# Kernel optimization log

Measured on AMD Instinct MI355X. Metric: run time of the kernel, lower is better.

The kernel has to match this reference:

```python
import jax, jax.numpy as jnp
import numpy as np

B, NQ, NK, C = 16, 8, 4096, 256
H = W = 64
HEADS = 8
CI = 128          # embedding_dim // attention_downsample_rate
HD = CI // HEADS  # per-head dim
EPS = float(np.finfo(np.float32).tiny)


def _gumbel_topk(scores, noise, n):
    # iterative gumbel-softmax top-k relaxation with straight-through hard k-hot
    g = scores + noise
    khot = jnp.zeros_like(g)
    onehot = jnp.zeros_like(g)
    for _ in range(n):
        g = g + jnp.log(jnp.maximum(1.0 - onehot, EPS))
        onehot = jax.nn.softmax(g, axis=-1)
        khot = khot + onehot
    _, ind = jax.lax.top_k(khot, n)
    rows = jnp.arange(khot.shape[0])[:, None]
    hard = jnp.zeros_like(khot).at[rows, ind].set(1.0)
    ret = hard - jax.lax.stop_gradient(khot) + khot  # == hard numerically
    return ret, jnp.sort(ind, axis=1)  # sorted idx = row-major order of boolean-mask select


def _sample_points(pe, content, ret, idx):
    # pe [H,W,C], content [b,H,W,C], ret [b,HW] k-hot, idx [b,k] sorted
    b = ret.shape[0]
    m = ret.reshape(b, H, W, 1)
    pe_m = (pe[None] * m).reshape(b, H * W, -1)
    c_m = (content * m).reshape(b, H * W, -1)
    take = lambda a: jnp.take_along_axis(a, idx[:, :, None], axis=1)
    return take(pe_m), take(c_m)


def _mlp(x, W1, b1, W2, b2, W3, b3):
    x = jax.nn.relu(x @ W1 + b1)
    x = jax.nn.relu(x @ W2 + b2)
    return x @ W3 + b3


def _forward(queries, keys, query_pe, key_pe, guiding_embedding, gumbel_p, gumbel_n,
             static_uncertain, static_refined, Wq, bq, Wk, bk, Wv, bv, Wo, bo,
             uW1, ub1, uW2, ub2, uW3, ub3, rW1, rb1, rW2, rb2, rW3, rb3,
             pe_gauss, point_pos, point_neg, n_sample_points):
    b = queries.shape[0]
    g = guiding_embedding.reshape(b, C, H * W).transpose(0, 2, 1)  # [b, HW, C]
    g = g * keys  # elementwise gating -> new guiding embedding

    # cross attention token -> image (internal dim CI, HEADS heads)
    def split_heads(x, Wx, bx):
        return (x @ Wx + bx).reshape(b, -1, HEADS, HD).transpose(0, 2, 1, 3)
    qh = split_heads(queries + query_pe, Wq, bq)
    kh = split_heads(g + key_pe, Wk, bk)
    vh = split_heads(g, Wv, bv)
    attn = jax.nn.softmax(jnp.einsum('bhqd,bhkd->bhqk', qh, kh) / np.float32(np.sqrt(HD)), axis=-1)
    out = jnp.einsum('bhqk,bhkd->bhqd', attn, vh).transpose(0, 2, 1, 3).reshape(b, -1, CI)
    queries = out @ Wo + bo  # [b, NQ, C]

    q1 = queries[:, 1, :]
    unc_tok = _mlp(jnp.concatenate([jnp.broadcast_to(static_uncertain, (b, C)), q1], -1),
                   uW1, ub1, uW2, ub2, uW3, ub3)
    ref_tok = _mlp(jnp.concatenate([jnp.broadcast_to(static_refined, (b, C)), q1], -1),
                   rW1, rb1, rW2, rb2, rW3, rb3)

    img = g.transpose(0, 2, 1)  # [b, C, HW]
    unc_norm = jax.nn.sigmoid(jnp.einsum('bc,bcn->bn', unc_tok, img))
    ref_mask = jnp.einsum('bc,bcn->bn', ref_tok, img)
    coarse_mask = jnp.einsum('bc,bcn->bn', q1, img)

    queries = jnp.concatenate([queries[:, 0:1], ref_tok[:, None, :], queries[:, 2:]], axis=1)

    # point-sampling reference map + gumbel-softmax top-k (training-path math)
    ref_map = unc_norm * (jax.nn.sigmoid(ref_mask) - jax.nn.sigmoid(coarse_mask))  # [b, HW]
    ret_p, idx_p = _gumbel_topk(ref_map, gumbel_p, n_sample_points)
    ret_n, idx_n = _gumbel_topk(-ref_map, gumbel_n, n_sample_points)

    # random fourier positional encoding of the 64x64 grid (SAM PositionEmbeddingRandom)
    xs = (jnp.arange(W, dtype=jnp.float32) + 0.5) / W
    ys = (jnp.arange(H, dtype=jnp.float32) + 0.5) / H
    coords = jnp.stack([jnp.tile(xs[None, :], (H, 1)), jnp.tile(ys[:, None], (1, W))], axis=-1)
    proj = ((2.0 * coords - 1.0) @ pe_gauss) * np.float32(2.0 * np.pi)  # [H, W, C//2]
    pe = jnp.concatenate([jnp.sin(proj), jnp.cos(proj)], axis=-1)       # [H, W, C]

    # F.interpolate of a 64x64 map to (64,64) is the identity here
    content = (keys + g).reshape(b, H, W, C)

    sp_pe, sp_c = _sample_points(pe, content, ret_p, idx_p)
    sn_pe, sn_c = _sample_points(pe, content, ret_n, idx_n)
    sp_pe = sp_pe + point_pos  # prompt_encoder.point_embeddings[1]
    sn_pe = sn_pe + point_neg  # prompt_encoder.point_embeddings[0]

    query_pe = jnp.concatenate([query_pe, sp_pe, sn_pe], axis=1)
    queries = jnp.concatenate([queries, sp_c, sn_c], axis=1)
    # pack (queries, query_pe) into one array for a single-output reference
    return jnp.concatenate([queries, query_pe], axis=1)  # [b, 2*(NQ+2k), C]


def setup_inputs():
    key = jax.random.key(0)
    ks = iter(jax.random.split(key, 48))
    n = lambda shape, s=1.0: jax.random.normal(next(ks), shape, jnp.float32) * s
    z = lambda shape: jnp.zeros(shape, jnp.float32)
    return {
        'queries': n((B, NQ, C)),
        'keys': n((B, NK, C)),
        'query_pe': n((B, NQ, C)),
        'key_pe': n((B, NK, C)),
        'guiding_embedding': n((B, C, H, W)),
        'gumbel_p': jax.random.gumbel(next(ks), (B, NK), jnp.float32),
        'gumbel_n': jax.random.gumbel(next(ks), (B, NK), jnp.float32),
        'static_uncertain': n((C,), 0.02),
        'static_refined': n((C,), 0.02),
        'Wq': n((C, CI), 0.02), 'bq': z((CI,)),
        'Wk': n((C, CI), 0.02), 'bk': z((CI,)),
        'Wv': n((C, CI), 0.02), 'bv': z((CI,)),
        'Wo': n((CI, C), 0.02), 'bo': z((C,)),
        'uW1': n((2 * C, C // 4), 0.05), 'ub1': z((C // 4,)),
        'uW2': n((C // 4, C // 4), 0.05), 'ub2': z((C // 4,)),
        'uW3': n((C // 4, C), 0.05), 'ub3': z((C,)),
        'rW1': n((2 * C, C // 4), 0.05), 'rb1': z((C // 4,)),
        'rW2': n((C // 4, C // 4), 0.05), 'rb2': z((C // 4,)),
        'rW3': n((C // 4, C), 0.05), 'rb3': z((C,)),
        'pe_gauss': n((2, C // 2)),
        'point_pos': n((C,), 0.02),
        'point_neg': n((C,), 0.02),
        'n_sample_points': 4,
    }


def reference(queries, keys, query_pe, key_pe, guiding_embedding, gumbel_p, gumbel_n,
              static_uncertain, static_refined, Wq, bq, Wk, bk, Wv, bv, Wo, bo,
              uW1, ub1, uW2, ub2, uW3, ub3, rW1, rb1, rW2, rb2, rW3, rb3,
              pe_gauss, point_pos, point_neg, n_sample_points):
    return _forward(queries, keys, query_pe, key_pe, guiding_embedding, gumbel_p, gumbel_n,
                    static_uncertain, static_refined, Wq, bq, Wk, bk, Wv, bv, Wo, bo,
                    uW1, ub1, uW2, ub2, uW3, ub3, rW1, rb1, rW2, rb2, rW3, rb3,
                    pe_gauss, point_pos, point_neg, n_sample_points)
```

## Files before the change

kernel.cpp:

```cpp
#include <hip/hip_runtime.h>

#define BB 16
#define NQn 8
#define NK 4096
#define CC 256
#define NHEADS 8
#define CIn 128
#define HDn 16
#define NHQ 64
#define EPS_TINY 1.17549435e-38f

constexpr size_t OFF_QK   = 0;
constexpr size_t OFF_QBK  = OFF_QK  + (size_t)BB*CC*NHQ;
constexpr size_t OFF_SC   = OFF_QBK + (size_t)BB*NHQ;
constexpr size_t OFF_MP   = OFF_SC  + (size_t)BB*NK*NHQ;
constexpr size_t OFF_SP   = OFF_MP  + (size_t)BB*32*NHQ;
constexpr size_t OFF_M    = OFF_SP  + (size_t)BB*32*NHQ;
constexpr size_t OFF_RS   = OFF_M   + (size_t)BB*NHQ;
constexpr size_t OFF_AVP  = OFF_RS  + (size_t)BB*NHQ;
constexpr size_t OFF_QATT = OFF_AVP + (size_t)BB*16*NHQ*CC;
constexpr size_t OFF_UNC  = OFF_QATT+ (size_t)BB*NQn*CC;
constexpr size_t OFF_REFT = OFF_UNC + (size_t)BB*CC;
constexpr size_t OFF_RMAP = OFF_REFT+ (size_t)BB*CC;
constexpr size_t OFF_IDX  = OFF_RMAP+ (size_t)BB*NK;
constexpr size_t OFF_RV   = OFF_IDX + 128;
constexpr size_t OFF_G    = OFF_RV  + 128;

__global__ __launch_bounds__(256) void k1_qside(
    const float* __restrict__ queries, const float* __restrict__ query_pe,
    const float* __restrict__ Wq, const float* __restrict__ bq,
    const float* __restrict__ Wk, const float* __restrict__ bk,
    float* __restrict__ ws)
{
  int b = blockIdx.x >> 3, q = blockIdx.x & 7, t = threadIdx.x;
  __shared__ float x[CC];
  __shared__ float qh[CIn];
  x[t] = queries[(b*NQn+q)*CC + t] + query_pe[(b*NQn+q)*CC + t];
  __syncthreads();
  if (t < CIn) {
    float a = bq[t];
    for (int c = 0; c < CC; ++c) a += x[c]*Wq[c*CIn + t];
    qh[t] = a * 0.25f;
  }
  __syncthreads();
  float* Qk = ws + OFF_QK;
  #pragma unroll
  for (int h = 0; h < NHEADS; ++h) {
    float a = 0.f;
    #pragma unroll
    for (int d = 0; d < HDn; ++d) a += qh[h*HDn+d] * Wk[t*CIn + h*HDn + d];
    Qk[((size_t)b*CC + t)*NHQ + h*NQn + q] = a;
  }
  if (t < NHEADS) {
    float a = 0.f;
    #pragma unroll
    for (int d = 0; d < HDn; ++d) a += qh[t*HDn+d] * bk[t*HDn+d];
    (ws + OFF_QBK)[b*NHQ + t*NQn + q] = a;
  }
}

__global__ __launch_bounds__(256, 8) void k2_scores(
    const float* __restrict__ keys, const float* __restrict__ key_pe,
    const float* __restrict__ guiding, float* __restrict__ ws)
{
  int b = blockIdx.y, n0 = blockIdx.x * 32, t = threadIdx.x;
  __shared__ __align__(16) float Xs[32][36];
  __shared__ __align__(16) float Qs[32][64];
  __shared__ float Gt[32][33];
  const float* Qk = ws + OFF_QK + (size_t)b*CC*NHQ;
  float* G = ws + OFF_G;
  const int tx = t & 15, ty = t >> 4;
  const int xr = t >> 3, xc4 = (t & 7) * 4;
  const int gn = t & 31, gc0 = (t >> 5) * 4;
  float acc[2][4] = {};

  float gld[4]; float4 kp, pp; float qp[8];
  {
    #pragma unroll
    for (int i = 0; i < 4; ++i)
      gld[i] = guiding[((size_t)b*CC + gc0 + i)*NK + n0 + gn];
    size_t kb = ((size_t)b*NK + n0 + xr)*CC + xc4;
    kp = *(const float4*)&keys[kb];
    pp = *(const float4*)&key_pe[kb];
    #pragma unroll
    for (int i = 0; i < 8; ++i) {
      int l = i*256 + t;
      qp[i] = Qk[(size_t)(l>>6)*NHQ + (l & 63)];
    }
  }
  for (int ch = 0; ch < 8; ++ch) {
    int c0 = ch*32;
    #pragma unroll
    for (int i = 0; i < 4; ++i) Gt[gc0 + i][gn] = gld[i];
    __syncthreads();
    #pragma unroll
    for (int i = 0; i < 8; ++i) {
      int l = i*256 + t;
      Qs[l>>6][l&63] = qp[i];
    }
    {
      size_t kbase = ((size_t)b*NK + n0 + xr)*CC + c0 + xc4;
      float4 g4;
      g4.x = kp.x * Gt[xc4+0][xr];
      g4.y = kp.y * Gt[xc4+1][xr];
      g4.z = kp.z * Gt[xc4+2][xr];
      g4.w = kp.w * Gt[xc4+3][xr];
      *(float4*)&G[kbase] = g4;
      float4 o; o.x=g4.x+pp.x; o.y=g4.y+pp.y; o.z=g4.z+pp.z; o.w=g4.w+pp.w;
      *(float4*)&Xs[xr][xc4] = o;
    }
    __syncthreads();
    if (ch < 7) {
      int c1 = c0 + 32;
      #pragma unroll
      for (int i = 0; i < 4; ++i)
        gld[i] = guiding[((size_t)b*CC + c1 + gc0 + i)*NK + n0 + gn];
      size_t kb2 = ((size_t)b*NK + n0 + xr)*CC + c1 + xc4;
      kp = *(const float4*)&keys[kb2];
      pp = *(const float4*)&key_pe[kb2];
      #pragma unroll
      for (int i = 0; i < 8; ++i) {
        int l = i*256 + t;
        qp[i] = Qk[(size_t)(c1 + (l>>6))*NHQ + (l & 63)];
      }
    }
    #pragma unroll
    for (int cb = 0; cb < 8; ++cb) {
      float4 x0 = *(const float4*)&Xs[2*ty][4*cb];
      float4 x1 = *(const float4*)&Xs[2*ty+1][4*cb];
      #pragma unroll
      for (int u = 0; u < 4; ++u) {
        float4 qf = *(const float4*)&Qs[4*cb+u][4*tx];
        float xu0 = ((const float*)&x0)[u];
        float xu1 = ((const float*)&x1)[u];
        acc[0][0] += xu0*qf.x; acc[0][1] += xu0*qf.y; acc[0][2] += xu0*qf.z; acc[0][3] += xu0*qf.w;
        acc[1][0] += xu1*qf.x; acc[1][1] += xu1*qf.y; acc[1][2] += xu1*qf.z; acc[1][3] += xu1*qf.w;
      }
    }
  }
  const float* qbk = ws + OFF_QBK + (size_t)b*NHQ;
  float qb[4] = {qbk[4*tx], qbk[4*tx+1], qbk[4*tx+2], qbk[4*tx+3]};
  float* sc = ws + OFF_SC + ((size_t)b*NK + n0)*NHQ;
  #pragma unroll
  for (int i = 0; i < 2; ++i) {
    float4 o;
    o.x = acc[i][0]+qb[0]; o.y = acc[i][1]+qb[1]; o.z = acc[i][2]+qb[2]; o.w = acc[i][3]+qb[3];
    *(float4*)&sc[(size_t)(2*ty + i)*NHQ + 4*tx] = o;
  }
}

__global__ __launch_bounds__(256) void k3a_stats(float* __restrict__ ws)
{
  int b = blockIdx.y, sb = blockIdx.x, t = threadIdx.x;
  int hq = t & 63, r = t >> 6;
  const float* sc = ws + OFF_SC + ((size_t)b*NK + sb*128)*NHQ;
  float m = -INFINITY, s = 0.f;
  for (int i = 0; i < 32; ++i) {
    float v = sc[(r + 4*i)*NHQ + hq];
    if (v > m) { s = s*expf(m - v) + 1.f; m = v; } else { s += expf(v - m); }
  }
  __shared__ float rm[256], rs[256];
  rm[t] = m; rs[t] = s;
  __syncthreads();
  if (t < 64) {
    float m0=rm[t], m1=rm[t+64], m2=rm[t+128], m3=rm[t+192];
    float mm = fmaxf(fmaxf(m0,m1), fmaxf(m2,m3));
    float ss = rs[t]*expf(m0-mm) + rs[t+64]*expf(m1-mm) + rs[t+128]*expf(m2-mm) + rs[t+192]*expf(m3-mm);
    (ws + OFF_MP)[(b*32 + sb)*NHQ + t] = mm;
    (ws + OFF_SP)[(b*32 + sb)*NHQ + t] = ss;
  }
}

__global__ __launch_bounds__(64) void k3b_combine(float* __restrict__ ws)
{
  int b = blockIdx.x, hq = threadIdx.x;
  const float* mp = ws + OFF_MP + (size_t)b*32*NHQ;
  const float* sp = ws + OFF_SP + (size_t)b*32*NHQ;
  float m = -INFINITY;
  #pragma unroll
  for (int i = 0; i < 32; ++i) m = fmaxf(m, mp[i*NHQ+hq]);
  float s = 0.f;
  #pragma unroll
  for (int i = 0; i < 32; ++i) s += sp[i*NHQ+hq]*expf(mp[i*NHQ+hq]-m);
  (ws+OFF_M)[b*NHQ+hq] = m;
  (ws+OFF_RS)[b*NHQ+hq] = 1.0f/s;
}

__global__ __launch_bounds__(256) void k3c_weights(float* __restrict__ ws)
{
  int b = blockIdx.y, t = threadIdx.x;
  size_t f = (size_t)blockIdx.x * 2048 + (size_t)t * 8;
  float* sc = ws + OFF_SC + (size_t)b*NK*NHQ + f;
  const float* m  = ws + OFF_M  + (size_t)b*NHQ;
  const float* rs = ws + OFF_RS + (size_t)b*NHQ;
  int hq0 = (int)(f & 63);
  float4 v0 = *(const float4*)&sc[0];
  float4 v1 = *(const float4*)&sc[4];
  float o[8] = {v0.x,v0.y,v0.z,v0.w, v1.x,v1.y,v1.z,v1.w};
  #pragma unroll
  for (int j = 0; j < 8; ++j) o[j] = expf(o[j] - m[hq0+j]) * rs[hq0+j];
  float4 w0; w0.x=o[0]; w0.y=o[1]; w0.z=o[2]; w0.w=o[3];
  float4 w1; w1.x=o[4]; w1.y=o[5]; w1.z=o[6]; w1.w=o[7];
  *(float4*)&sc[0] = w0;
  *(float4*)&sc[4] = w1;
}

__global__ __launch_bounds__(256, 8) void k4_av(float* __restrict__ ws)
{
  int xb = blockIdx.x, cq = blockIdx.y, b = blockIdx.z, t = threadIdx.x;
  int kb = xb >> 1, hh = (xb & 1) * 32;
  int k0 = kb * 256, cbase = cq * 64;
  __shared__ __align__(16) float gld[32][68];
  __shared__ __align__(16) float wld[32][36];
  const int hq0 = (t & 7) * 4, c0 = (t >> 3) * 2;
  const int sr = t >> 4, sc4 = (t & 15) * 4;
  float acc[4][2] = {};
  const float* Wp = ws + OFF_SC;
  const float* G  = ws + OFF_G;
  for (int kk = 0; kk < 256; kk += 32) {
    __syncthreads();
    #pragma unroll
    for (int p = 0; p < 2; ++p)
      *(float4*)&gld[p*16 + sr][sc4] =
        *(const float4*)&G[((size_t)b*NK + k0+kk + p*16 + sr)*CC + cbase + sc4];
    #pragma unroll
    for (int i = 0; i < 4; ++i) {
      int l = i*256 + t; int k = l >> 5, hqw = l & 31;
      wld[k][hqw] = Wp[((size_t)b*NK + k0+kk+k)*NHQ + hh + hqw];
    }
    __syncthreads();
    #pragma unroll 4
    for (int k = 0; k < 32; ++k) {
      float4 w4 = *(const float4*)&wld[k][hq0];
      float2 g2 = *(const float2*)&gld[k][c0];
      acc[0][0] += w4.x*g2.x; acc[0][1] += w4.x*g2.y;
      acc[1][0] += w4.y*g2.x; acc[1][1] += w4.y*g2.y;
      acc[2][0] += w4.z*g2.x; acc[2][1] += w4.z*g2.y;
      acc[3][0] += w4.w*g2.x; acc[3][1] += w4.w*g2.y;
    }
  }
  float* avp = ws + OFF_AVP + (((size_t)b*16 + kb)*NHQ + hh + hq0)*CC + cbase + c0;
  #pragma unroll
  for (int i = 0; i < 4; ++i)
    *(float2*)&avp[(size_t)i*CC] = make_float2(acc[i][0], acc[i][1]);
}

__global__ __launch_bounds__(256) void k56_attout(
    const float* __restrict__ Wv, const float* __restrict__ bv,
    const float* __restrict__ Wo, const float* __restrict__ bo,
    float* __restrict__ ws)
{
  int b = blockIdx.x >> 3, q = blockIdx.x & 7, t = threadIdx.x;
  __shared__ float avs[NHEADS][CC];
  __shared__ float outv[CIn];
  const float* avp = ws + OFF_AVP;
  #pragma unroll
  for (int h = 0; h < NHEADS; ++h) {
    int hq = h*NQn + q;
    float a = 0.f;
    #pragma unroll 4
    for (int kb = 0; kb < 16; ++kb)
      a += avp[(((size_t)b*16 + kb)*NHQ + hq)*CC + t];
    avs[h][t] = a;
  }
  __syncthreads();
  if (t < CIn) {
    int h = t >> 4;
    float a = bv[t];
    for (int c = 0; c < CC; ++c) a += avs[h][c]*Wv[c*CIn + t];
    outv[t] = a;
  }
  __syncthreads();
  float a = bo[t];
  for (int ci = 0; ci < CIn; ++ci) a += outv[ci]*Wo[ci*CC + t];
  (ws+OFF_QATT)[((size_t)b*NQn + q)*CC + t] = a;
}

__global__ __launch_bounds__(256) void k7_mlps(
    const float* __restrict__ su, const float* __restrict__ sr,
    const float* __restrict__ uW1, const float* __restrict__ ub1,
    const float* __restrict__ uW2, const float* __restrict__ ub2,
    const float* __restrict__ uW3, const float* __restrict__ ub3,
    const float* __restrict__ rW1, const float* __restrict__ rb1,
    const float* __restrict__ rW2, const float* __restrict__ rb2,
    const float* __restrict__ rW3, const float* __restrict__ rb3,
    float* __restrict__ ws)
{
  int b = blockIdx.x, t = threadIdx.x;
  __shared__ float xs[768];
  __shared__ float h1[2][64], h2[2][64];
  xs[t] = su[t];
  xs[256+t] = (ws+OFF_QATT)[((size_t)b*NQn + 1)*CC + t];
  xs[512+t] = sr[t];
  __syncthreads();
  if (t < 128) {
    int which = t >> 6, o = t & 63;
    const float* W1 = which ? rW1 : uW1;
    const float* b1 = which ? rb1 : ub1;
    int base = which ? 512 : 0;
    float a = b1[o];
    for (int i = 0; i < 256; ++i) a += xs[base+i]*W1[i*64 + o];
    for (int i = 0; i < 256; ++i) a += xs[256+i]*W1[(256+i)*64 + o];
    h1[which][o] = fmaxf(a, 0.f);
  }
  __syncthreads();
  if (t < 128) {
    int which = t >> 6, o = t & 63;
    const float* W2 = which ? rW2 : uW2;
    const float* b2 = which ? rb2 : ub2;
    float a = b2[o];
    #pragma unroll 8
    for (int i = 0; i < 64; ++i) a += h1[which][i]*W2[i*64+o];
    h2[which][o] = fmaxf(a, 0.f);
  }
  __syncthreads();
  {
    float a = ub3[t];
    #pragma unroll 8
    for (int i = 0; i < 64; ++i) a += h2[0][i]*uW3[i*CC + t];
    (ws+OFF_UNC)[b*CC + t] = a;
    float a2 = rb3[t];
    #pragma unroll 8
    for (int i = 0; i < 64; ++i) a2 += h2[1][i]*rW3[i*CC + t];
    (ws+OFF_REFT)[b*CC + t] = a2;
  }
}

__global__ __launch_bounds__(256) void k8_masks(float* __restrict__ ws)
{
  int b = blockIdx.y, t = threadIdx.x;
  int wave = t >> 6, lane = t & 63;
  __shared__ float q1s[CC], us[CC], rts[CC];
  q1s[t] = (ws+OFF_QATT)[((size_t)b*NQn+1)*CC + t];
  us[t]  = (ws+OFF_UNC)[b*CC + t];
  rts[t] = (ws+OFF_REFT)[b*CC + t];
  __syncthreads();
  float q1v[4], usv[4], rtv[4];
  #pragma unroll
  for (int u = 0; u < 4; ++u) {
    q1v[u] = q1s[lane*4+u]; usv[u] = us[lane*4+u]; rtv[u] = rts[lane*4+u];
  }
  const float* G = ws + OFF_G;
  float* rmap = ws + OFF_RMAP + (size_t)b*NK;
  int n_base = blockIdx.x*32 + wave*8;
  for (int r = 0; r < 8; ++r) {
    int n = n_base + r;
    float4 gv = *(const float4*)&G[((size_t)b*NK + n)*CC + lane*4];
    float aq = gv.x*q1v[0] + gv.y*q1v[1] + gv.z*q1v[2] + gv.w*q1v[3];
    float au = gv.x*usv[0] + gv.y*usv[1] + gv.z*usv[2] + gv.w*usv[3];
    float ar = gv.x*rtv[0] + gv.y*rtv[1] + gv.z*rtv[2] + gv.w*rtv[3];
    #pragma unroll
    for (int s = 1; s < 64; s <<= 1) {
      aq += __shfl_xor(aq, s, 64);
      au += __shfl_xor(au, s, 64);
      ar += __shfl_xor(ar, s, 64);
    }
    if (lane == 0) {
      float un = 1.f/(1.f+expf(-au));
      rmap[n] = un * (1.f/(1.f+expf(-ar)) - 1.f/(1.f+expf(-aq)));
    }
  }
}

__global__ __launch_bounds__(256) void k9_gumbel(
    const float* __restrict__ gp, const float* __restrict__ gn,
    float* __restrict__ ws)
{
  int sign = blockIdx.x, b = blockIdx.y, t = threadIdx.x;
  int wave = t >> 6, lane = t & 63;
  const float* noise = sign ? gn : gp;
  const float* rmap = ws + OFF_RMAP + (size_t)b*NK;
  float g[16], kh[16], oh[16];
  #pragma unroll
  for (int i = 0; i < 16; ++i) {
    int n = i*256 + t;
    float scv = rmap[n];
    if (sign) scv = -scv;
    g[i] = scv + noise[(size_t)b*NK + n];
    kh[i] = 0.f; oh[i] = 0.f;
  }
  __shared__ float wred[8];
  __shared__ float selV[16];
  __shared__ int   selIdx[16];
  for (int it = 0; it < 4; ++it) {
    if (it > 0) {
      #pragma unroll
      for (int i = 0; i < 16; ++i) g[i] += logf(fmaxf(1.f - oh[i], EPS_TINY));
    }
    float m = g[0];
    #pragma unroll
    for (int i = 1; i < 16; ++i) m = fmaxf(m, g[i]);
    #pragma unroll
    for (int s = 1; s < 64; s <<= 1) m = fmaxf(m, __shfl_xor(m, s, 64));
    if (lane == 0) wred[wave] = m;
    __syncthreads();
    m = fmaxf(fmaxf(wred[0], wred[1]), fmaxf(wred[2], wred[3]));
    float e[16], ls = 0.f;
    #pragma unroll
    for (int i = 0; i < 16; ++i) { e[i] = expf(g[i]-m); ls += e[i]; }
    #pragma unroll
    for (int s = 1; s < 64; s <<= 1) ls += __shfl_xor(ls, s, 64);
    if (lane == 0) wred[4+wave] = ls;
    __syncthreads();
    float ssum = wred[4]+wred[5]+wred[6]+wred[7];
    #pragma unroll
    for (int i = 0; i < 16; ++i) { oh[i] = e[i]/ssum; kh[i] += oh[i]; }
  }
  int id[4]; float rr[4];
  for (int j = 0; j < 4; ++j) {
    float bv = kh[0]; int bi = t;
    #pragma unroll
    for (int i = 1; i < 16; ++i) {
      if (kh[i] > bv) { bv = kh[i]; bi = i*256 + t; }
    }
    #pragma unroll
    for (int s = 1; s < 64; s <<= 1) {
      float ov = __shfl_xor(bv, s, 64);
      int   oi = __shfl_xor(bi, s, 64);
      if (ov > bv || (ov == bv && oi < bi)) { bv = ov; bi = oi; }
    }
    if (lane == 0) { selV[j*4+wave] = bv; selIdx[j*4+wave] = bi; }
    __syncthreads();
    bv = selV[j*4]; bi = selIdx[j*4];
    #pragma unroll
    for (int w = 1; w < 4; ++w) {
      float ov = selV[j*4+w]; int oi = selIdx[j*4+w];
      if (ov > bv || (ov == bv && oi < bi)) { bv = ov; bi = oi; }
    }
    id[j] = bi; rr[j] = (1.f - bv) + bv;
    if ((bi & 255) == t) kh[bi >> 8] = -1.f;
  }
  if (t == 0) {
    for (int a = 0; a < 3; ++a)
      for (int c2 = a+1; c2 < 4; ++c2)
        if (id[c2] < id[a]) { int ti=id[a]; id[a]=id[c2]; id[c2]=ti; float tr=rr[a]; rr[a]=rr[c2]; rr[c2]=tr; }
    int* iout = (int*)(ws + OFF_IDX);
    float* rout = ws + OFF_RV;
    for (int j = 0; j < 4; ++j) {
      iout[(sign*BB + b)*4 + j] = id[j];
      rout[(sign*BB + b)*4 + j] = rr[j];
    }
  }
}

__global__ __launch_bounds__(256) void k10_out(
    const float* __restrict__ keys, const float* __restrict__ query_pe,
    const float* __restrict__ point_pos, const float* __restrict__ point_neg,
    const float* __restrict__ pe_gauss,
    float* __restrict__ ws, float* __restrict__ out)
{
  int b = blockIdx.y, r = blockIdx.x, t = threadIdx.x;
  const float* G = ws + OFF_G;
  float val;
  if (r < 8) {
    val = (r == 1) ? (ws+OFF_REFT)[b*CC + t]
                   : (ws+OFF_QATT)[((size_t)b*NQn + r)*CC + t];
  } else if (r < 16) {
    int j = r - 8; int sign = j >> 2; int jj = j & 3;
    int idx = ((const int*)(ws+OFF_IDX))[(sign*BB + b)*4 + jj];
    float rvv = (ws+OFF_RV)[(sign*BB + b)*4 + jj];
    float kv = keys[((size_t)b*NK + idx)*CC + t];
    float gv = G[((size_t)b*NK + idx)*CC + t];
    val = (kv + gv) * rvv;
  } else if (r < 24) {
    val = query_pe[((size_t)b*NQn + (r-16))*CC + t];
  } else {
    int j = r - 24; int sign = j >> 2; int jj = j & 3;
    int idx = ((const int*)(ws+OFF_IDX))[(sign*BB + b)*4 + jj];
    float rvv = (ws+OFF_RV)[(sign*BB + b)*4 + jj];
    const float* point = sign ? point_neg : point_pos;
    int h = idx >> 6, w = idx & 63;
    float x = (w + 0.5f)/64.f, y = (h + 0.5f)/64.f;
    int jf = (t < 128) ? t : (t - 128);
    float proj = ((2.f*x - 1.f)*pe_gauss[jf] + (2.f*y - 1.f)*pe_gauss[128 + jf]) * 6.28318530717958647692f;
    float sv = (t < 128) ? sinf(proj) : cosf(proj);
    val = sv*rvv + point[t];
  }
  out[((size_t)b*32 + r)*CC + t] = val;
}

extern "C" void kernel_launch(void* const* d_in, const int* in_sizes, int n_in,
                              void* d_out, int out_size, void* d_ws, size_t ws_size,
                              hipStream_t stream)
{
  const float* queries   = (const float*)d_in[0];
  const float* keys      = (const float*)d_in[1];
  const float* query_pe  = (const float*)d_in[2];
  const float* key_pe    = (const float*)d_in[3];
  const float* guiding   = (const float*)d_in[4];
  const float* gumbel_p  = (const float*)d_in[5];
  const float* gumbel_n  = (const float*)d_in[6];
  const float* s_unc     = (const float*)d_in[7];
  const float* s_ref     = (const float*)d_in[8];
  const float* Wq  = (const float*)d_in[9];   const float* bq  = (const float*)d_in[10];
  const float* Wk  = (const float*)d_in[11];  const float* bk  = (const float*)d_in[12];
  const float* Wv  = (const float*)d_in[13];  const float* bv  = (const float*)d_in[14];
  const float* Wo  = (const float*)d_in[15];  const float* bo  = (const float*)d_in[16];
  const float* uW1 = (const float*)d_in[17];  const float* ub1 = (const float*)d_in[18];
  const float* uW2 = (const float*)d_in[19];  const float* ub2 = (const float*)d_in[20];
  const float* uW3 = (const float*)d_in[21];  const float* ub3 = (const float*)d_in[22];
  const float* rW1 = (const float*)d_in[23];  const float* rb1 = (const float*)d_in[24];
  const float* rW2 = (const float*)d_in[25];  const float* rb2 = (const float*)d_in[26];
  const float* rW3 = (const float*)d_in[27];  const float* rb3 = (const float*)d_in[28];
  const float* pe_gauss  = (const float*)d_in[29];
  const float* point_pos = (const float*)d_in[30];
  const float* point_neg = (const float*)d_in[31];
  float* ws = (float*)d_ws;
  float* out = (float*)d_out;

  k1_qside  <<<dim3(BB*NQn),    256, 0, stream>>>(queries, query_pe, Wq, bq, Wk, bk, ws);
  k2_scores <<<dim3(128, BB),   256, 0, stream>>>(keys, key_pe, guiding, ws);
  k3a_stats <<<dim3(32, BB),    256, 0, stream>>>(ws);
  k3b_combine<<<dim3(BB),        64, 0, stream>>>(ws);
  k3c_weights<<<dim3(128, BB),  256, 0, stream>>>(ws);
  k4_av     <<<dim3(32, 4, BB), 256, 0, stream>>>(ws);
  k56_attout<<<dim3(BB*NQn),    256, 0, stream>>>(Wv, bv, Wo, bo, ws);
  k7_mlps   <<<dim3(BB),        256, 0, stream>>>(s_unc, s_ref, uW1, ub1, uW2, ub2, uW3, ub3,
                                                  rW1, rb1, rW2, rb2, rW3, rb3, ws);
  k8_masks  <<<dim3(128, BB),   256, 0, stream>>>(ws);
  k9_gumbel <<<dim3(2, BB),     256, 0, stream>>>(gumbel_p, gumbel_n, ws);
  k10_out   <<<dim3(32, BB),    256, 0, stream>>>(keys, query_pe, point_pos, point_neg,
                                                  pe_gauss, ws, out);
}
```

Measured before the change: 250.9 us.

## Fuse softmax normalization into AV kernel and widen per-thread tile

Removes the separate k3c_weights pass that rewrote the full score buffer with normalized exponentials. k4_av now computes exp(s-m)*rs on the fly while loading scores into shared memory, so one read-write pass over the 16x4096x64 score buffer and one launch go away. The AV block also covers all 64 head-query columns with a 4x4 per-thread register tile instead of 4x2 over half the columns, which halves the grid and increases reuse. The trade-off is that each exp is recomputed four times, once per channel-quarter block, and occupancy may drop since the 8-block launch bound hint is gone.

```diff
diff --git a/kernel.cpp b/kernel.cpp
--- a/kernel.cpp
+++ b/kernel.cpp
@@ -186,63 +186,52 @@
   (ws+OFF_RS)[b*NHQ+hq] = 1.0f/s;
 }
 
-__global__ __launch_bounds__(256) void k3c_weights(float* __restrict__ ws)
-{
-  int b = blockIdx.y, t = threadIdx.x;
-  size_t f = (size_t)blockIdx.x * 2048 + (size_t)t * 8;
-  float* sc = ws + OFF_SC + (size_t)b*NK*NHQ + f;
-  const float* m  = ws + OFF_M  + (size_t)b*NHQ;
-  const float* rs = ws + OFF_RS + (size_t)b*NHQ;
-  int hq0 = (int)(f & 63);
-  float4 v0 = *(const float4*)&sc[0];
-  float4 v1 = *(const float4*)&sc[4];
-  float o[8] = {v0.x,v0.y,v0.z,v0.w, v1.x,v1.y,v1.z,v1.w};
-  #pragma unroll
-  for (int j = 0; j < 8; ++j) o[j] = expf(o[j] - m[hq0+j]) * rs[hq0+j];
-  float4 w0; w0.x=o[0]; w0.y=o[1]; w0.z=o[2]; w0.w=o[3];
-  float4 w1; w1.x=o[4]; w1.y=o[5]; w1.z=o[6]; w1.w=o[7];
-  *(float4*)&sc[0] = w0;
-  *(float4*)&sc[4] = w1;
-}
-
-__global__ __launch_bounds__(256, 8) void k4_av(float* __restrict__ ws)
-{
-  int xb = blockIdx.x, cq = blockIdx.y, b = blockIdx.z, t = threadIdx.x;
-  int kb = xb >> 1, hh = (xb & 1) * 32;
-  int k0 = kb * 256, cbase = cq * 64;
+__global__ __launch_bounds__(256) void k4_av(float* __restrict__ ws)
+{
+  int kb = blockIdx.x, ch = blockIdx.y, b = blockIdx.z, t = threadIdx.x;
+  int k0 = kb * 256, cbase = ch * 64;
   __shared__ __align__(16) float gld[32][68];
-  __shared__ __align__(16) float wld[32][36];
-  const int hq0 = (t & 7) * 4, c0 = (t >> 3) * 2;
-  const int sr = t >> 4, sc4 = (t & 15) * 4;
-  float acc[4][2] = {};
-  const float* Wp = ws + OFF_SC;
+  __shared__ __align__(16) float wld[32][64];
+  __shared__ float mv[64], rv[64];
+  if (t < 64) { mv[t] = (ws+OFF_M)[b*NHQ+t]; rv[t] = (ws+OFF_RS)[b*NHQ+t]; }
+  int hq0 = (t & 15) * 4, c0 = (t >> 4) * 4;
+  int sr = t >> 4, sc4 = (t & 15) * 4;
+  float accf[4][4] = {};
+  const float* sc = ws + OFF_SC;
   const float* G  = ws + OFF_G;
+  __syncthreads();
   for (int kk = 0; kk < 256; kk += 32) {
-    __syncthreads();
     #pragma unroll
     for (int p = 0; p < 2; ++p)
       *(float4*)&gld[p*16 + sr][sc4] =
         *(const float4*)&G[((size_t)b*NK + k0+kk + p*16 + sr)*CC + cbase + sc4];
     #pragma unroll
-    for (int i = 0; i < 4; ++i) {
-      int l = i*256 + t; int k = l >> 5, hqw = l & 31;
-      wld[k][hqw] = Wp[((size_t)b*NK + k0+kk+k)*NHQ + hh + hqw];
+    for (int i = 0; i < 8; ++i) {
+      int l = i*256 + t; int k = l >> 6, hq = l & 63;
+      float v = sc[((size_t)b*NK + k0+kk+k)*NHQ + hq];
+      wld[k][hq] = expf(v - mv[hq]) * rv[hq];
     }
     __syncthreads();
     #pragma unroll 4
     for (int k = 0; k < 32; ++k) {
       float4 w4 = *(const float4*)&wld[k][hq0];
-      float2 g2 = *(const float2*)&gld[k][c0];
-      acc[0][0] += w4.x*g2.x; acc[0][1] += w4.x*g2.y;
-      acc[1][0] += w4.y*g2.x; acc[1][1] += w4.y*g2.y;
-      acc[2][0] += w4.z*g2.x; acc[2][1] += w4.z*g2.y;
-      acc[3][0] += w4.w*g2.x; acc[3][1] += w4.w*g2.y;
-    }
-  }
-  float* avp = ws + OFF_AVP + (((size_t)b*16 + kb)*NHQ + hh + hq0)*CC + cbase + c0;
-  #pragma unroll
-  for (int i = 0; i < 4; ++i)
-    *(float2*)&avp[(size_t)i*CC] = make_float2(acc[i][0], acc[i][1]);
+      float4 gv = *(const float4*)&gld[k][c0];
+      float wq[4] = {w4.x, w4.y, w4.z, w4.w};
+      float gq[4] = {gv.x, gv.y, gv.z, gv.w};
+      #pragma unroll
+      for (int i = 0; i < 4; ++i)
+        #pragma unroll
+        for (int j = 0; j < 4; ++j) accf[i][j] += wq[i]*gq[j];
+    }
+    __syncthreads();
+  }
+  float* avp = ws + OFF_AVP + (((size_t)b*16 + kb)*NHQ)*CC;
+  #pragma unroll
+  for (int i = 0; i < 4; ++i) {
+    float4 o;
+    o.x = accf[i][0]; o.y = accf[i][1]; o.z = accf[i][2]; o.w = accf[i][3];
+    *(float4*)&avp[(size_t)(hq0 + i)*CC + cbase + c0] = o;
+  }
 }
 
 __global__ __launch_bounds__(256) void k56_attout(
@@ -512,8 +501,7 @@
   k2_scores <<<dim3(128, BB),   256, 0, stream>>>(keys, key_pe, guiding, ws);
   k3a_stats <<<dim3(32, BB),    256, 0, stream>>>(ws);
   k3b_combine<<<dim3(BB),        64, 0, stream>>>(ws);
-  k3c_weights<<<dim3(128, BB),  256, 0, stream>>>(ws);
-  k4_av     <<<dim3(32, 4, BB), 256, 0, stream>>>(ws);
+  k4_av     <<<dim3(16, 4, BB), 256, 0, stream>>>(ws);
   k56_attout<<<dim3(BB*NQn),    256, 0, stream>>>(Wv, bv, Wo, bo, ws);
   k7_mlps   <<<dim3(BB),        256, 0, stream>>>(s_unc, s_ref, uW1, ub1, uW2, ub2, uW3, ub3,
                                                   rW1, rb1, rW2, rb2, rW3, rb3, ws);
```

Measured after the change: 231.4 us. -7.8%, faster.
